# Kernel tuning notes

Measured on AMD Instinct MI355X. Metric: run time of the kernel, lower is better.

## Reference

```python
import jax, jax.numpy as jnp
import numpy as np

IN_DIM = 768
OUT_DIM = 768


def setup_inputs() -> dict:
    key = jax.random.key(0)
    k_x, k_q, k_k, k_v = jax.random.split(key, 4)
    B, S = 4, 4096
    x = jax.random.normal(k_x, (B, S, IN_DIM), dtype=jnp.float32)
    scale = 1.0 / np.sqrt(IN_DIM)
    Wq = jax.random.normal(k_q, (IN_DIM, OUT_DIM), dtype=jnp.float32) * scale
    Wk = jax.random.normal(k_k, (IN_DIM, OUT_DIM), dtype=jnp.float32) * scale
    Wv = jax.random.normal(k_v, (IN_DIM, OUT_DIM), dtype=jnp.float32) * scale
    return {"x": x, "Wq": Wq, "Wk": Wk, "Wv": Wv}


def reference(x, Wq, Wk, Wv):
    # x: [B, S, D_in]; W*: [D_in, D_out] (Linear without bias)
    q = jnp.einsum('bsd,de->bse', x, Wq)
    k = jnp.einsum('bsd,de->bse', x, Wk)
    v = jnp.einsum('bsd,de->bse', x, Wv)
    S = x.shape[1]
    scores = jnp.einsum('bqe,bke->bqk', q, k)  # [B, S, S]
    causal = jnp.tril(jnp.ones((S, S), dtype=bool))  # True where allowed
    scores = jnp.where(causal[None], scores, -jnp.inf)
    scale = 1.0 / jnp.sqrt(jnp.asarray(q.shape[-1], dtype=scores.dtype))
    weights = jax.nn.softmax(scores * scale, axis=-1)
    # dropout p=0.0 -> identity
    return jnp.einsum('bqk,bke->bqe', weights, v)
```

## Files before the change

kernel.cpp:

```cpp
#include <hip/hip_runtime.h>
#include <hip/hip_bf16.h>
#include <hip/hip_fp16.h>

#define DIM 768
#define SLEN 4096
#define BATCH 4
#define NTILES 528
#define NT256 136
#define SPB ((size_t)NTILES * 16384)

typedef __attribute__((ext_vector_type(8))) short short8;
typedef __attribute__((ext_vector_type(4))) short short4v;
typedef __attribute__((ext_vector_type(4))) float f32x4;
typedef __attribute__((ext_vector_type(8))) _Float16 f16x8;

typedef __attribute__((address_space(1))) void gvoid;
typedef __attribute__((address_space(3))) void lvoid;

__device__ __forceinline__ void gl_lds16(const void* g, void* l) {
  __builtin_amdgcn_global_load_lds((gvoid*)g, (lvoid*)l, 16, 0, 0);
}

__device__ __forceinline__ unsigned short f2h(float x) {
  union { _Float16 h; unsigned short u; } c; c.h = (_Float16)x; return c.u;
}
__device__ __forceinline__ float h2f(unsigned short u) {
  union { _Float16 h; unsigned short u; } c; c.u = u; return (float)c.h;
}

union V8 { short8 v; unsigned short u[8]; };

__global__ __launch_bounds__(256) void convert_x_kernel(
    const float* __restrict__ x, unsigned short* __restrict__ xb) {
  size_t i = ((size_t)blockIdx.x * 256 + threadIdx.x) * 8;
  f32x4 a = *(const f32x4*)(x + i);
  f32x4 b = *(const f32x4*)(x + i + 4);
  V8 o;
#pragma unroll
  for (int j = 0; j < 4; ++j) { o.u[j] = f2h(a[j]); o.u[4 + j] = f2h(b[j]); }
  *(short8*)(xb + i) = o.v;
}

__global__ __launch_bounds__(256) void transpose_w_kernel(
    const float* __restrict__ Wq, const float* __restrict__ Wk,
    const float* __restrict__ Wv, unsigned short* __restrict__ Wt) {
  __shared__ float Tl[32][33];
  const float* Wi = blockIdx.z == 0 ? Wq : (blockIdx.z == 1 ? Wk : Wv);
  unsigned short* Wo = Wt + (size_t)blockIdx.z * DIM * DIM;
  int k0 = blockIdx.x * 32, n0 = blockIdx.y * 32;
  int t = threadIdx.x;
  int r = t >> 3, c4 = (t & 7) * 4;
  f32x4 v = *(const f32x4*)(Wi + (size_t)(k0 + r) * DIM + n0 + c4);
#pragma unroll
  for (int j = 0; j < 4; ++j) Tl[r][c4 + j] = v[j];
  __syncthreads();
  short4v ov;
#pragma unroll
  for (int j = 0; j < 4; ++j) ov[j] = (short)f2h(Tl[c4 + j][r]);
  *(short4v*)(Wo + (size_t)(n0 + r) * DIM + k0 + c4) = ov;
}


#define STAGE(src, row0, kb, ldsoff)                                              \
  {                                                                               \
    gl_lds16((src) + (size_t)((row0) + rA) * DIM + (kb) + cA,                     \
             ldsb + (ldsoff) + t * 16);                                           \
    gl_lds16((src) + (size_t)((row0) + 64 + rA) * DIM + (kb) + cA,                \
             ldsb + (ldsoff) + 8192 + t * 16);                                    \
  }

#define STAGEP(srcp, stride, ldsoff)                                              \
  {                                                                               \
    gl_lds16((srcp) + (size_t)rA * (stride) + cA, ldsb + (ldsoff) + t * 16);      \
    gl_lds16((srcp) + (size_t)(64 + rA) * (stride) + cA,                          \
             ldsb + (ldsoff) + 8192 + t * 16);                                    \
  }

#define QPHASE(MH, CHB, STG, VMW)                                                 \
  {                                                                               \
    f16x8 afr[4];                                                                 \
    _Pragma("unroll") for (int j = 0; j < 4; ++j)                                 \
        afr[j] = __builtin_bit_cast(f16x8, *(const short8*)(ldsb + aB +           \
                 (MH) * 16384 + (j * 32 + arow) * 128 + (CHB)));                  \
    if ((MH) == 0) {                                                              \
      _Pragma("unroll") for (int n = 0; n < 4; ++n)                               \
          bfr[n] = __builtin_bit_cast(f16x8, *(const short8*)(ldsb + bB +         \
                   bh * 16384 + (brow + n * 16) * 128 + (CHB)));                  \
    }                                                                             \
    STG;                                                                          \
    VMW;                                                                          \
    asm volatile("s_barrier" ::: "memory");                                       \
    asm volatile("s_waitcnt lgkmcnt(0)" ::: "memory");                            \
    __builtin_amdgcn_sched_barrier(0);                                            \
    __builtin_amdgcn_s_setprio(1);                                                \
    _Pragma("unroll") for (int j = 0; j < 4; ++j)                                 \
      _Pragma("unroll") for (int n = 0; n < 4; ++n)                               \
        acc[(MH) * 4 + j][n] = __builtin_amdgcn_mfma_f32_16x16x32_f16(            \
            afr[j], bfr[n], acc[(MH) * 4 + j][n], 0, 0, 0);                       \
    __builtin_amdgcn_s_setprio(0);                                                \
    __builtin_amdgcn_sched_barrier(0);                                            \
    asm volatile("s_barrier" ::: "memory");                                       \
  }

template <int MODE>
__global__ __launch_bounds__(512, 2) void gemm8_kernel(
    const unsigned short* __restrict__ Ag, const unsigned short* __restrict__ Bg,
    unsigned short* __restrict__ o0, unsigned short* __restrict__ o1,
    size_t stAB, size_t stS) {
  __shared__ __align__(16) unsigned short lds[65536];
  char* ldsb = (char*)lds;
  const int t = threadIdx.x;
  const int lane = t & 63, w = t >> 6;
  const int l15 = lane & 15, lg = lane >> 4;
  const int wr = w >> 2, wc = w & 3;

  int m0, n0, qt = 0, kt = 0;
  const unsigned short *A, *B;
  unsigned short* Co = nullptr;
  unsigned short* Sb = nullptr;
  if (MODE == 0) {
    m0 = blockIdx.x * 256; n0 = blockIdx.y * 256;
    A = Ag; B = Bg + (size_t)blockIdx.z * DIM * DIM;
    Co = blockIdx.z == 0 ? o0 : o1;
  } else if (MODE == 2) {
    m0 = blockIdx.y * 256; n0 = blockIdx.x * 256;
    A = Ag; B = Bg;
    Co = o0;
  } else {
    const int i = blockIdx.x, b = blockIdx.y;
    qt = (int)((sqrtf(8.f * i + 1.f) - 1.f) * 0.5f);
    while ((qt + 1) * (qt + 2) / 2 <= i) ++qt;
    while (qt * (qt + 1) / 2 > i) --qt;
    kt = i - qt * (qt + 1) / 2;
    m0 = qt * 256; n0 = kt * 256;
    A = Ag + (size_t)b * stAB; B = Bg + (size_t)b * stAB;
    Sb = o0 + (size_t)b * stS;
  }

  const int rA = t >> 3;
  const int cA = (((t & 7) ^ ((t >> 3) & 7)) << 3);
  const int ch0 = ((lg ^ (l15 & 7)) << 4);
  const int arow = wr * 16 + l15;
  const int bh = wc >> 1;
  const int brow = (wc & 1) * 64 + l15;

  f32x4 acc[8][4];
#pragma unroll
  for (int f = 0; f < 8; ++f)
#pragma unroll
    for (int n = 0; n < 4; ++n) acc[f][n] = f32x4{0.f, 0.f, 0.f, 0.f};

  STAGE(A, m0, 0, 0);
  STAGE(B, n0, 0, 65536);
  STAGE(B, n0 + 128, 0, 65536 + 16384);
  STAGE(A, m0 + 128, 0, 16384);
  STAGE(A, m0, 64, 32768);
  asm volatile("s_waitcnt vmcnt(4)" ::: "memory");
  asm volatile("s_barrier" ::: "memory");

  for (int tt = 0; tt < 12; ++tt) {
    const int bt = tt & 1;
    const int aB = bt * 32768;
    const int bB = 65536 + bt * 32768;
    const int aN = (1 - bt) * 32768;
    const int bN = 65536 + (1 - bt) * 32768;
    const int kb1 = (tt + 1 < 12 ? tt + 1 : 11) * 64;
    const int kb2 = (tt + 2 < 12 ? tt + 2 : 11) * 64;
    f16x8 bfr[4];
    QPHASE(0, ch0, STAGE(B, n0, kb1, bN),
           asm volatile("s_waitcnt vmcnt(4)" ::: "memory"));
    QPHASE(1, ch0, STAGE(B, n0 + 128, kb1, bN + 16384), (void)0);
    QPHASE(0, ch0 ^ 64, STAGE(A, m0 + 128, kb1, aN + 16384), (void)0);
    QPHASE(1, ch0 ^ 64, STAGE(A, m0, kb2, aB),
           asm volatile("s_waitcnt vmcnt(4)" ::: "memory"));
  }
  asm volatile("s_waitcnt vmcnt(0)" ::: "memory");

  if (MODE == 0) {
#pragma unroll
    for (int f = 0; f < 8; ++f) {
      const int row = m0 + f * 32 + wr * 16 + lg * 4;
#pragma unroll
      for (int n = 0; n < 4; ++n) {
        const int col = n0 + wc * 64 + n * 16 + l15;
#pragma unroll
        for (int ii = 0; ii < 4; ++ii)
          Co[(size_t)(row + ii) * DIM + col] = f2h(acc[f][n][ii]);
      }
    }
  } else if (MODE == 2) {
    const int bb = n0 >> 12;
    unsigned short* O = Co + (size_t)bb * DIM * SLEN;
#pragma unroll
    for (int f = 0; f < 8; ++f) {
      const int row = m0 + f * 32 + wr * 16 + lg * 4;
#pragma unroll
      for (int n = 0; n < 4; ++n) {
        const int sl = (n0 + wc * 64 + n * 16 + l15) & (SLEN - 1);
#pragma unroll
        for (int ii = 0; ii < 4; ++ii)
          O[(size_t)(row + ii) * SLEN + sl] = f2h(acc[f][n][ii]);
      }
    }
  } else {
#pragma unroll
    for (int f = 0; f < 8; ++f) {
      const int rl = (f * 32 + wr * 16 + lg * 4) & 127;
      const int Q128 = qt * 2 + (f >= 4 ? 1 : 0);
      const int K128 = kt * 2 + (wc >> 1);
      if (K128 > Q128) continue;
      const size_t tb = (size_t)(Q128 * (Q128 + 1) / 2 + K128) * 16384;
#pragma unroll
      for (int n = 0; n < 4; ++n) {
        const int cl = ((wc & 1) * 64 + n * 16 + l15);
#pragma unroll
        for (int ii = 0; ii < 4; ++ii)
          Sb[tb + (size_t)(rl + ii) * 128 + cl] = f2h(acc[f][n][ii]);
      }
    }
  }
}

__global__ __launch_bounds__(256) void softmax_kernel(
    unsigned short* __restrict__ S, size_t s_bstride) {
  __shared__ float redm[4], reds[4];
  const int r = blockIdx.x, b = blockIdx.y;
  unsigned short* Sb = S + (size_t)b * s_bstride;
  const int qt = r >> 7, rl = r & 127;
  const int ncols = (qt + 1) * 128;
  const size_t rowbase = (size_t)(qt * (qt + 1) / 2) * 16384 + (size_t)rl * 128;
  const int t = threadIdx.x, lane = t & 63, w = t >> 6;
  const int c0 = t * 16;
  const bool act = c0 < ncols;
  const float NEG = -3.0e38f;
  float sv[16];
  unsigned short* p = nullptr;
  if (act) {
    int ktile = c0 >> 7, cl = c0 & 127;
    p = Sb + rowbase + (size_t)ktile * 16384 + cl;
    V8 v0, v1; v0.v = *(const short8*)p; v1.v = *(const short8*)(p + 8);
#pragma unroll
    for (int j = 0; j < 8; ++j) {
      sv[j] = (c0 + j > r) ? NEG : h2f(v0.u[j]);
      sv[8 + j] = (c0 + 8 + j > r) ? NEG : h2f(v1.u[j]);
    }
  } else {
#pragma unroll
    for (int j = 0; j < 16; ++j) sv[j] = NEG;
  }
  float mx = NEG;
#pragma unroll
  for (int j = 0; j < 16; ++j) mx = fmaxf(mx, sv[j]);
#pragma unroll
  for (int d = 1; d < 64; d <<= 1) mx = fmaxf(mx, __shfl_xor(mx, d));
  if (lane == 0) redm[w] = mx;
  __syncthreads();
  mx = fmaxf(fmaxf(redm[0], redm[1]), fmaxf(redm[2], redm[3]));
  const float scl = 1.4426950408889634f / 27.712812921102035f;
  float e[16], sm = 0.f;
#pragma unroll
  for (int j = 0; j < 16; ++j) { e[j] = exp2f((sv[j] - mx) * scl); sm += e[j]; }
#pragma unroll
  for (int d = 1; d < 64; d <<= 1) sm += __shfl_xor(sm, d);
  if (lane == 0) reds[w] = sm;
  __syncthreads();
  float inv = 1.0f / (reds[0] + reds[1] + reds[2] + reds[3]);
  if (act) {
    V8 o0, o1;
#pragma unroll
    for (int j = 0; j < 8; ++j) { o0.u[j] = f2h(e[j] * inv); o1.u[j] = f2h(e[8 + j] * inv); }
    *(short8*)p = o0.v;
    *(short8*)(p + 8) = o1.v;
  }
}

__global__ __launch_bounds__(256) void zero_tile_kernel(unsigned short* __restrict__ z) {
  ((short8*)z)[blockIdx.x * 256 + threadIdx.x] = short8{0, 0, 0, 0, 0, 0, 0, 0};
}

__device__ const int pv_mt[24]  = {15,15,7,14,14,13,13,6,12,12,11,11,5,10,10,9,9,4,8,8,3,2,1,0};
__device__ const int pv_ks0[24] = {0,32,0,0,30,0,28,0,0,26,0,24,0,0,22,0,20,0,0,18,0,0,0,0};
__device__ const int pv_kl[24]  = {32,32,32,30,30,28,28,28,26,26,24,24,24,22,22,20,20,20,18,18,16,12,8,4};
__device__ const int pv_sec[24] = {0,1,0,0,1,0,1,0,0,1,0,1,0,0,1,0,1,0,0,1,0,0,0,0};

__global__ __launch_bounds__(512, 2) void pv256_kernel(
    const unsigned short* __restrict__ S, const unsigned short* __restrict__ Vt,
    const unsigned short* __restrict__ Zt, float* __restrict__ Out,
    float* __restrict__ Part) {
  __shared__ __align__(16) unsigned short lds[65536];
  char* ldsb = (char*)lds;
  const int t = threadIdx.x, lane = t & 63, w = t >> 6;
  const int l15 = lane & 15, lg = lane >> 4;
  const int wr = w >> 2, wc = w & 3;
  const int rank = blockIdx.x / 12, sub = blockIdx.x % 12;
  const int b = sub / 3, nt = sub % 3;
  const int mt = pv_mt[rank], ks0 = pv_ks0[rank], kl = pv_kl[rank];
  const int sec = pv_sec[rank];
  const int q0 = 2 * mt, q1 = 2 * mt + 1;
  const int kend = ks0 + kl;
  const unsigned short* Sbb = S + (size_t)b * SPB;
  const unsigned short* Vb = Vt + (size_t)b * DIM * SLEN + (size_t)(nt * 256) * SLEN;

  auto asrc = [&](int ks, int qh) -> const unsigned short* {
    const int K128 = ks >> 1;
    const unsigned short* base =
        (K128 <= qh) ? Sbb + (size_t)(qh * (qh + 1) / 2 + K128) * 16384 : Zt;
    return base + (ks & 1) * 64;
  };

  const int rA = t >> 3;
  const int cA = (((t & 7) ^ ((t >> 3) & 7)) << 3);
  const int ch0 = ((lg ^ (l15 & 7)) << 4);
  const int arow = wr * 16 + l15;
  const int bh = wc >> 1;
  const int brow = (wc & 1) * 64 + l15;

  f32x4 acc[8][4];
#pragma unroll
  for (int f = 0; f < 8; ++f)
#pragma unroll
    for (int n = 0; n < 4; ++n) acc[f][n] = f32x4{0.f, 0.f, 0.f, 0.f};

  const int ksp = (ks0 + 1 < kend) ? ks0 + 1 : kend - 1;
  STAGEP(asrc(ks0, q0), 128, 0);
  STAGEP(Vb + (size_t)ks0 * 64, SLEN, 65536);
  STAGEP(Vb + (size_t)128 * SLEN + (size_t)ks0 * 64, SLEN, 65536 + 16384);
  STAGEP(asrc(ks0, q1), 128, 16384);
  STAGEP(asrc(ksp, q0), 128, 32768);
  asm volatile("s_waitcnt vmcnt(4)" ::: "memory");
  asm volatile("s_barrier" ::: "memory");

  for (int it = 0; it < kl; ++it) {
    const int ts = ks0 + it;
    const int bt = it & 1;
    const int aB = bt * 32768;
    const int bB = 65536 + bt * 32768;
    const int aN = (1 - bt) * 32768;
    const int bN = 65536 + (1 - bt) * 32768;
    const int t1 = (ts + 1 < kend) ? ts + 1 : kend - 1;
    const int t2 = (ts + 2 < kend) ? ts + 2 : kend - 1;
    f16x8 bfr[4];
    QPHASE(0, ch0, STAGEP(Vb + (size_t)t1 * 64, SLEN, bN),
           asm volatile("s_waitcnt vmcnt(4)" ::: "memory"));
    QPHASE(1, ch0, STAGEP(Vb + (size_t)128 * SLEN + (size_t)t1 * 64, SLEN, bN + 16384),
           (void)0);
    QPHASE(0, ch0 ^ 64, STAGEP(asrc(t1, q1), 128, aN + 16384), (void)0);
    QPHASE(1, ch0 ^ 64, STAGEP(asrc(t2, q0), 128, aB),
           asm volatile("s_waitcnt vmcnt(4)" ::: "memory"));
  }
  asm volatile("s_waitcnt vmcnt(0)" ::: "memory");

  if (!sec) {
    float* Ob = Out + (size_t)b * SLEN * DIM + (size_t)(mt * 256) * DIM + nt * 256;
#pragma unroll
    for (int f = 0; f < 8; ++f) {
      const int rl = f * 32 + wr * 16 + lg * 4;
#pragma unroll
      for (int n = 0; n < 4; ++n) {
        const int cl = wc * 64 + n * 16 + l15;
#pragma unroll
        for (int ii = 0; ii < 4; ++ii)
          Ob[(size_t)(rl + ii) * DIM + cl] = acc[f][n][ii];
      }
    }
  } else {
    float* Pb = Part + (size_t)((b * 3 + nt) * 8 + (mt - 8)) * 65536;
#pragma unroll
    for (int f = 0; f < 8; ++f) {
      const int rl = f * 32 + wr * 16 + lg * 4;
#pragma unroll
      for (int n = 0; n < 4; ++n) {
        const int cl = wc * 64 + n * 16 + l15;
#pragma unroll
        for (int ii = 0; ii < 4; ++ii)
          Pb[(size_t)(rl + ii) * 256 + cl] = acc[f][n][ii];
      }
    }
  }
}

__global__ __launch_bounds__(256) void pv_reduce_kernel(
    const float* __restrict__ Part, float* __restrict__ Out) {
  const int bx = blockIdx.x;
  const int p = bx >> 6;
  const int within = ((bx & 63) * 256 + threadIdx.x) * 4;
  const int mt = 8 + (p & 7);
  const int bnt = p >> 3, b = bnt / 3, nt = bnt % 3;
  const int r = within >> 8, c = within & 255;
  float* o = Out + (size_t)b * SLEN * DIM + (size_t)(mt * 256 + r) * DIM + nt * 256 + c;
  const f32x4 pv = *(const f32x4*)(Part + (size_t)p * 65536 + within);
  const f32x4 ov = *(const f32x4*)o;
  *(f32x4*)o = ov + pv;
}

__global__ __launch_bounds__(256) void gemm_pv_kernel(
    const unsigned short* __restrict__ S, const unsigned short* __restrict__ Vt,
    float* __restrict__ Out, size_t s_bstride, int nb) {
  __shared__ __align__(16) unsigned short As[4096], Bs[4096];
  const int idx = blockIdx.x;
  const int qtr = idx / (6 * nb);
  const int rem = idx - qtr * 6 * nb;
  const int b = rem / 6, nt = rem % 6;
  const int qt = 31 - qtr;
  const unsigned short* Sb = S + (size_t)b * s_bstride + (size_t)(qt * (qt + 1) / 2) * 16384;
  const unsigned short* Vb = Vt + (size_t)b * DIM * SLEN + (size_t)(nt * 128) * SLEN;
  float* Ob = Out + (size_t)b * SLEN * DIM + (size_t)(qt * 128) * DIM + nt * 128;
  const int t = threadIdx.x, lane = t & 63, w = t >> 6;
  const int l15 = lane & 15, lg = lane >> 4;
  const int wm = w >> 1, wn = w & 1;
  f32x4 acc[4][4];
#pragma unroll
  for (int a = 0; a < 4; ++a)
#pragma unroll
    for (int b2 = 0; b2 < 4; ++b2) acc[a][b2] = f32x4{0.f, 0.f, 0.f, 0.f};
  const int c0 = t, c1 = t + 256;
  const int r0 = c0 >> 2, k80 = (c0 & 3) * 8;
  const int r1 = c1 >> 2, k81 = (c1 & 3) * 8;
  const int ksteps = (qt + 1) * 4;
  for (int ks = 0; ks < ksteps; ++ks) {
    const int kb = ks * 32;
    const size_t atile = (size_t)(kb >> 7) * 16384 + (size_t)(kb & 127);
    __syncthreads();
    gl_lds16(Sb + atile + (size_t)r0 * 128 + k80, As + (size_t)c0 * 8);
    gl_lds16(Sb + atile + (size_t)r1 * 128 + k81, As + (size_t)c1 * 8);
    gl_lds16(Vb + (size_t)r0 * SLEN + kb + k80, Bs + (size_t)c0 * 8);
    gl_lds16(Vb + (size_t)r1 * SLEN + kb + k81, Bs + (size_t)c1 * 8);
    __syncthreads();
    f16x8 a[4], bf[4];
#pragma unroll
    for (int mi = 0; mi < 4; ++mi)
      a[mi] = __builtin_bit_cast(f16x8, *(const short8*)(As + (wm * 64 + mi * 16 + l15) * 32 + lg * 8));
#pragma unroll
    for (int ni = 0; ni < 4; ++ni)
      bf[ni] = __builtin_bit_cast(f16x8, *(const short8*)(Bs + (wn * 64 + ni * 16 + l15) * 32 + lg * 8));
#pragma unroll
    for (int mi = 0; mi < 4; ++mi)
#pragma unroll
      for (int ni = 0; ni < 4; ++ni)
        acc[mi][ni] = __builtin_amdgcn_mfma_f32_16x16x32_f16(a[mi], bf[ni], acc[mi][ni], 0, 0, 0);
  }
#pragma unroll
  for (int mi = 0; mi < 4; ++mi)
#pragma unroll
    for (int ni = 0; ni < 4; ++ni)
#pragma unroll
      for (int ii = 0; ii < 4; ++ii) {
        int rl = wm * 64 + mi * 16 + lg * 4 + ii;
        int cl = wn * 64 + ni * 16 + l15;
        Ob[(size_t)rl * DIM + cl] = acc[mi][ni][ii];
      }
}

extern "C" void kernel_launch(void* const* d_in, const int* in_sizes, int n_in,
                              void* d_out, int out_size, void* d_ws, size_t ws_size,
                              hipStream_t stream) {
  const float* x  = (const float*)d_in[0];
  const float* Wq = (const float*)d_in[1];
  const float* Wk = (const float*)d_in[2];
  const float* Wv = (const float*)d_in[3];
  float* out = (float*)d_out;

  const size_t n_x = (size_t)BATCH * SLEN * DIM;
  unsigned short* Q  = (unsigned short*)d_ws;
  unsigned short* K  = Q + n_x;
  unsigned short* Vt = K + n_x;
  unsigned short* xb = Vt + n_x;
  unsigned short* wt = xb + n_x;
  const size_t base_elems = 4 * n_x + (size_t)3 * DIM * DIM;
  const bool full = ws_size >= (base_elems + 4 * SPB) * 2;

  convert_x_kernel<<<dim3((unsigned)(n_x / 8 / 256)), 256, 0, stream>>>(x, xb);
  transpose_w_kernel<<<dim3(DIM / 32, DIM / 32, 3), 256, 0, stream>>>(Wq, Wk, Wv, wt);

  gemm8_kernel<0><<<dim3(64, 3, 2), 512, 0, stream>>>(xb, wt, Q, K, 0, 0);
  gemm8_kernel<2><<<dim3(64, 3), 512, 0, stream>>>(
      wt + (size_t)2 * DIM * DIM, xb, Vt, nullptr, 0, 0);

  if (full) {
    unsigned short* S = (unsigned short*)d_ws + base_elems;
    zero_tile_kernel<<<8, 256, 0, stream>>>(wt);
    gemm8_kernel<1><<<dim3(NT256, BATCH), 512, 0, stream>>>(
        Q, K, S, nullptr, (size_t)SLEN * DIM, SPB);
    softmax_kernel<<<dim3(SLEN, BATCH), 256, 0, stream>>>(S, SPB);
    pv256_kernel<<<dim3(288), 512, 0, stream>>>(S, Vt, wt, out, (float*)xb);
    pv_reduce_kernel<<<dim3(6144), 256, 0, stream>>>((const float*)xb, out);
  } else {
    unsigned short* S = xb;
    for (int b = 0; b < BATCH; ++b) {
      const size_t qo = (size_t)b * SLEN * DIM;
      gemm8_kernel<1><<<dim3(NT256, 1), 512, 0, stream>>>(
          Q + qo, K + qo, S, nullptr, 0, 0);
      softmax_kernel<<<dim3(SLEN, 1), 256, 0, stream>>>(S, 0);
      gemm_pv_kernel<<<dim3(32 * 6), 256, 0, stream>>>(
          S, Vt + (size_t)b * DIM * SLEN, out + qo, 0, 1);
    }
  }
}
```

Baseline: 298.8 us.

## Merge QKV projection launches, swizzle block order, and regroup prefetch stages

Fuses the Q/K projection launch and the transposed V projection launch into one 576-block grid, with an XCD-aware block index remap so neighbouring tiles share the L2 of the same chiplet. The QK^T launch gets the same remap. In both the projection GEMM and the PV kernel, the prefetch pipeline issues two tile loads in the first and last phases instead of one per phase, and B is now also prefetched two stages ahead. This trades evenly spread memory issue for larger load bursts, and the deeper B prefetch relies on the existing double-buffered LDS layout.

```diff
diff --git a/kernel.cpp b/kernel.cpp
--- a/kernel.cpp
+++ b/kernel.cpp
@@ -106,7 +106,7 @@
 __global__ __launch_bounds__(512, 2) void gemm8_kernel(
     const unsigned short* __restrict__ Ag, const unsigned short* __restrict__ Bg,
     unsigned short* __restrict__ o0, unsigned short* __restrict__ o1,
-    size_t stAB, size_t stS) {
+    unsigned short* __restrict__ o2, size_t stAB, size_t stS) {
   __shared__ __align__(16) unsigned short lds[65536];
   char* ldsb = (char*)lds;
   const int t = threadIdx.x;
@@ -114,20 +114,28 @@
   const int l15 = lane & 15, lg = lane >> 4;
   const int wr = w >> 2, wc = w & 3;
 
-  int m0, n0, qt = 0, kt = 0;
+  int m0, n0, qt = 0, kt = 0, z = 0;
   const unsigned short *A, *B;
   unsigned short* Co = nullptr;
   unsigned short* Sb = nullptr;
   if (MODE == 0) {
-    m0 = blockIdx.x * 256; n0 = blockIdx.y * 256;
-    A = Ag; B = Bg + (size_t)blockIdx.z * DIM * DIM;
-    Co = blockIdx.z == 0 ? o0 : o1;
-  } else if (MODE == 2) {
-    m0 = blockIdx.y * 256; n0 = blockIdx.x * 256;
-    A = Ag; B = Bg;
-    Co = o0;
+    const int o = blockIdx.x;
+    const int oi = (o & 7) * 72 + (o >> 3);
+    const int mt = oi / 9, sub = oi - mt * 9;
+    const int ntile = sub / 3;
+    z = sub - ntile * 3;
+    if (z < 2) {
+      m0 = mt * 256; n0 = ntile * 256;
+      A = Ag; B = Bg + (size_t)z * DIM * DIM;
+      Co = z == 0 ? o0 : o1;
+    } else {
+      m0 = ntile * 256; n0 = mt * 256;
+      A = Bg + (size_t)2 * DIM * DIM; B = Ag;
+      Co = o2;
+    }
   } else {
-    const int i = blockIdx.x, b = blockIdx.y;
+    const int i0 = blockIdx.x, b = blockIdx.y;
+    const int i = (i0 & 7) * 17 + (i0 >> 3);
     qt = (int)((sqrtf(8.f * i + 1.f) - 1.f) * 0.5f);
     while ((qt + 1) * (qt + 2) / 2 <= i) ++qt;
     while (qt * (qt + 1) / 2 > i) --qt;
@@ -154,6 +162,7 @@
   STAGE(B, n0, 0, 65536);
   STAGE(B, n0 + 128, 0, 65536 + 16384);
   STAGE(A, m0 + 128, 0, 16384);
+  STAGE(B, n0, 64, 65536 + 32768);
   STAGE(A, m0, 64, 32768);
   asm volatile("s_waitcnt vmcnt(4)" ::: "memory");
   asm volatile("s_barrier" ::: "memory");
@@ -167,39 +176,43 @@
     const int kb1 = (tt + 1 < 12 ? tt + 1 : 11) * 64;
     const int kb2 = (tt + 2 < 12 ? tt + 2 : 11) * 64;
     f16x8 bfr[4];
-    QPHASE(0, ch0, STAGE(B, n0, kb1, bN),
+    QPHASE(0, ch0,
+           STAGE(B, n0 + 128, kb1, bN + 16384); STAGE(A, m0 + 128, kb1, aN + 16384),
+           (void)0);
+    QPHASE(1, ch0, (void)0, (void)0);
+    QPHASE(0, ch0 ^ 64, (void)0, (void)0);
+    QPHASE(1, ch0 ^ 64,
+           STAGE(B, n0, kb2, bB); STAGE(A, m0, kb2, aB),
            asm volatile("s_waitcnt vmcnt(4)" ::: "memory"));
-    QPHASE(1, ch0, STAGE(B, n0 + 128, kb1, bN + 16384), (void)0);
-    QPHASE(0, ch0 ^ 64, STAGE(A, m0 + 128, kb1, aN + 16384), (void)0);
-    QPHASE(1, ch0 ^ 64, STAGE(A, m0, kb2, aB),
-           asm volatile("s_waitcnt vmcnt(4)" ::: "memory"));
   }
   asm volatile("s_waitcnt vmcnt(0)" ::: "memory");
 
   if (MODE == 0) {
-#pragma unroll
-    for (int f = 0; f < 8; ++f) {
-      const int row = m0 + f * 32 + wr * 16 + lg * 4;
-#pragma unroll
-      for (int n = 0; n < 4; ++n) {
-        const int col = n0 + wc * 64 + n * 16 + l15;
-#pragma unroll
-        for (int ii = 0; ii < 4; ++ii)
-          Co[(size_t)(row + ii) * DIM + col] = f2h(acc[f][n][ii]);
+    if (z < 2) {
+#pragma unroll
+      for (int f = 0; f < 8; ++f) {
+        const int row = m0 + f * 32 + wr * 16 + lg * 4;
+#pragma unroll
+        for (int n = 0; n < 4; ++n) {
+          const int col = n0 + wc * 64 + n * 16 + l15;
+#pragma unroll
+          for (int ii = 0; ii < 4; ++ii)
+            Co[(size_t)(row + ii) * DIM + col] = f2h(acc[f][n][ii]);
+        }
       }
-    }
-  } else if (MODE == 2) {
-    const int bb = n0 >> 12;
-    unsigned short* O = Co + (size_t)bb * DIM * SLEN;
-#pragma unroll
-    for (int f = 0; f < 8; ++f) {
-      const int row = m0 + f * 32 + wr * 16 + lg * 4;
-#pragma unroll
-      for (int n = 0; n < 4; ++n) {
-        const int sl = (n0 + wc * 64 + n * 16 + l15) & (SLEN - 1);
-#pragma unroll
-        for (int ii = 0; ii < 4; ++ii)
-          O[(size_t)(row + ii) * SLEN + sl] = f2h(acc[f][n][ii]);
+    } else {
+      const int bb = n0 >> 12;
+      unsigned short* O = Co + (size_t)bb * DIM * SLEN;
+#pragma unroll
+      for (int f = 0; f < 8; ++f) {
+        const int row = m0 + f * 32 + wr * 16 + lg * 4;
+#pragma unroll
+        for (int n = 0; n < 4; ++n) {
+          const int sl = (n0 + wc * 64 + n * 16 + l15) & (SLEN - 1);
+#pragma unroll
+          for (int ii = 0; ii < 4; ++ii)
+            O[(size_t)(row + ii) * SLEN + sl] = f2h(acc[f][n][ii]);
+        }
       }
     }
   } else {
@@ -326,6 +339,7 @@
   STAGEP(Vb + (size_t)ks0 * 64, SLEN, 65536);
   STAGEP(Vb + (size_t)128 * SLEN + (size_t)ks0 * 64, SLEN, 65536 + 16384);
   STAGEP(asrc(ks0, q1), 128, 16384);
+  STAGEP(Vb + (size_t)ksp * 64, SLEN, 65536 + 32768);
   STAGEP(asrc(ksp, q0), 128, 32768);
   asm volatile("s_waitcnt vmcnt(4)" ::: "memory");
   asm volatile("s_barrier" ::: "memory");
@@ -340,12 +354,15 @@
     const int t1 = (ts + 1 < kend) ? ts + 1 : kend - 1;
     const int t2 = (ts + 2 < kend) ? ts + 2 : kend - 1;
     f16x8 bfr[4];
-    QPHASE(0, ch0, STAGEP(Vb + (size_t)t1 * 64, SLEN, bN),
-           asm volatile("s_waitcnt vmcnt(4)" ::: "memory"));
-    QPHASE(1, ch0, STAGEP(Vb + (size_t)128 * SLEN + (size_t)t1 * 64, SLEN, bN + 16384),
+    QPHASE(0, ch0,
+           STAGEP(Vb + (size_t)128 * SLEN + (size_t)t1 * 64, SLEN, bN + 16384);
+           STAGEP(asrc(t1, q1), 128, aN + 16384),
            (void)0);
-    QPHASE(0, ch0 ^ 64, STAGEP(asrc(t1, q1), 128, aN + 16384), (void)0);
-    QPHASE(1, ch0 ^ 64, STAGEP(asrc(t2, q0), 128, aB),
+    QPHASE(1, ch0, (void)0, (void)0);
+    QPHASE(0, ch0 ^ 64, (void)0, (void)0);
+    QPHASE(1, ch0 ^ 64,
+           STAGEP(Vb + (size_t)t2 * 64, SLEN, bB);
+           STAGEP(asrc(t2, q0), 128, aB),
            asm volatile("s_waitcnt vmcnt(4)" ::: "memory"));
   }
   asm volatile("s_waitcnt vmcnt(0)" ::: "memory");
@@ -472,15 +489,13 @@
   convert_x_kernel<<<dim3((unsigned)(n_x / 8 / 256)), 256, 0, stream>>>(x, xb);
   transpose_w_kernel<<<dim3(DIM / 32, DIM / 32, 3), 256, 0, stream>>>(Wq, Wk, Wv, wt);
 
-  gemm8_kernel<0><<<dim3(64, 3, 2), 512, 0, stream>>>(xb, wt, Q, K, 0, 0);
-  gemm8_kernel<2><<<dim3(64, 3), 512, 0, stream>>>(
-      wt + (size_t)2 * DIM * DIM, xb, Vt, nullptr, 0, 0);
+  gemm8_kernel<0><<<dim3(576), 512, 0, stream>>>(xb, wt, Q, K, Vt, 0, 0);
 
   if (full) {
     unsigned short* S = (unsigned short*)d_ws + base_elems;
     zero_tile_kernel<<<8, 256, 0, stream>>>(wt);
     gemm8_kernel<1><<<dim3(NT256, BATCH), 512, 0, stream>>>(
-        Q, K, S, nullptr, (size_t)SLEN * DIM, SPB);
+        Q, K, S, nullptr, nullptr, (size_t)SLEN * DIM, SPB);
     softmax_kernel<<<dim3(SLEN, BATCH), 256, 0, stream>>>(S, SPB);
     pv256_kernel<<<dim3(288), 512, 0, stream>>>(S, Vt, wt, out, (float*)xb);
     pv_reduce_kernel<<<dim3(6144), 256, 0, stream>>>((const float*)xb, out);
@@ -489,7 +504,7 @@
     for (int b = 0; b < BATCH; ++b) {
       const size_t qo = (size_t)b * SLEN * DIM;
       gemm8_kernel<1><<<dim3(NT256, 1), 512, 0, stream>>>(
-          Q + qo, K + qo, S, nullptr, 0, 0);
+          Q + qo, K + qo, S, nullptr, nullptr, 0, 0);
       softmax_kernel<<<dim3(SLEN, 1), 256, 0, stream>>>(S, 0);
       gemm_pv_kernel<<<dim3(32 * 6), 256, 0, stream>>>(
           S, Vt + (size_t)b * DIM * SLEN, out + qo, 0, 1);
```

Measured after the change: 294.4 us. Within noise of the previous version (-1.5%).
